# Kernel optimization log

Measured on AMD Instinct MI355X. Metric: run time of the kernel, lower is better.

## Reference

```python
import jax, jax.numpy as jnp
import numpy as np

B, T = 64, 2048
DEC, ENC, ATT, LOC, K = 1024, 512, 128, 32, 31


def setup_inputs() -> dict:
    key = jax.random.key(0)
    ks = jax.random.split(key, 9)
    inv = lambda n: 1.0 / np.sqrt(n)
    return {
        "query": jax.random.normal(ks[0], (B, DEC), dtype=jnp.float32),
        "values": jax.random.normal(ks[1], (B, T, ENC), dtype=jnp.float32),
        "cumulative_attention_weights": jax.random.uniform(ks[2], (B, T), dtype=jnp.float32),
        "mask": jnp.zeros((B, T), dtype=bool),
        "Q_w": jax.random.uniform(ks[3], (ATT, DEC), jnp.float32, -inv(DEC), inv(DEC)),
        "Q_b": jax.random.uniform(ks[4], (ATT,), jnp.float32, -inv(DEC), inv(DEC)),
        "V_w": jax.random.uniform(ks[5], (ATT, ENC), jnp.float32, -inv(ENC), inv(ENC)),
        "conv_w": jax.random.uniform(ks[6], (LOC, 1, K), jnp.float32, -inv(K), inv(K)),
        "loc_proj_w": jax.random.uniform(ks[7], (ATT, LOC), jnp.float32, -inv(LOC), inv(LOC)),
        "v_w": jax.random.uniform(ks[8], (1, ATT), jnp.float32, -inv(ATT), inv(ATT)),
    }


def reference(query, values, cumulative_attention_weights, mask,
              Q_w, Q_b, V_w, conv_w, loc_proj_w, v_w):
    # query projection: [B, 1, ATT] (broadcast over T)
    q = query @ Q_w.T + Q_b                       # [B, ATT]
    q = q[:, None, :]
    # values cache: [B, T, ATT]
    v_cache = jnp.einsum("bte,ae->bta", values, V_w)
    # location features: Conv1d(1 -> LOC, k=31, same padding) over cum weights
    x = cumulative_attention_weights[:, None, :]   # [B, 1, T]
    loc = jax.lax.conv_general_dilated(
        x, conv_w, window_strides=(1,), padding="SAME",
        dimension_numbers=("NCH", "OIH", "NCH"))   # [B, LOC, T]
    loc = jnp.einsum("bct,ac->bta", loc, loc_proj_w)  # [B, T, ATT]
    # additive attention energies
    energies = jnp.tanh(q + v_cache + loc) @ v_w[0]   # [B, T]
    energies = jnp.where(mask, -jnp.inf, energies)
    attention_weights = jax.nn.softmax(energies, axis=1)
    # context: [B, ENC]
    attention_context = jnp.einsum("bt,bte->be", attention_weights, values)
    return attention_context, attention_weights
```

## Files before the change

kernel.cpp:

```cpp
#include <hip/hip_runtime.h>
#include <hip/hip_bf16.h>
#include <math.h>

#define B_  64
#define T_  2048
#define DEC_ 1024
#define ENC_ 512
#define ATT_ 128
#define LOC_ 32
#define KW_  31

typedef __attribute__((ext_vector_type(8))) short short8;
typedef __attribute__((ext_vector_type(4))) float f32x4;
typedef __attribute__((ext_vector_type(4))) unsigned int u32x4;

__device__ inline unsigned short bf16_rn(float x) {
    unsigned int u = __builtin_bit_cast(unsigned int, x);
    unsigned int r = u + 0x7fffu + ((u >> 16) & 1u);
    return (unsigned short)(r >> 16);
}
__device__ inline float bf16_to_f(unsigned short h) {
    unsigned int u = ((unsigned int)h) << 16;
    return __builtin_bit_cast(float, u);
}

__device__ inline void cvt_split8_exact(const float* f, short8& hi8, short8& lo8) {
    u32x4 hw, lw;
    #pragma unroll
    for (int p = 0; p < 4; ++p) {
        float a = f[2 * p], b2 = f[2 * p + 1];
        unsigned u0 = __builtin_bit_cast(unsigned, a);
        unsigned u1 = __builtin_bit_cast(unsigned, b2);
        unsigned r0 = u0 + 0x7fffu + ((u0 >> 16) & 1u);
        unsigned r1 = u1 + 0x7fffu + ((u1 >> 16) & 1u);
        hw[p] = (r0 >> 16) | (r1 & 0xffff0000u);
        float d0 = a  - __builtin_bit_cast(float, r0 & 0xffff0000u);
        float d1 = b2 - __builtin_bit_cast(float, r1 & 0xffff0000u);
        unsigned v0 = __builtin_bit_cast(unsigned, d0);
        unsigned v1 = __builtin_bit_cast(unsigned, d1);
        unsigned s0 = v0 + 0x7fffu + ((v0 >> 16) & 1u);
        unsigned s1 = v1 + 0x7fffu + ((v1 >> 16) & 1u);
        lw[p] = (s0 >> 16) | (s1 & 0xffff0000u);
    }
    hi8 = __builtin_bit_cast(short8, hw);
    lo8 = __builtin_bit_cast(short8, lw);
}

__global__ __launch_bounds__(256) void prep_kernel(
    const float* __restrict__ query, const float* __restrict__ Q_w,
    const float* __restrict__ Q_b, const float* __restrict__ conv_w,
    const float* __restrict__ loc_proj_w, const float* __restrict__ V_w,
    float* __restrict__ qbuf, unsigned short* __restrict__ Bpk,
    unsigned short* __restrict__ effh, unsigned short* __restrict__ effl)
{
    int bi = blockIdx.x, tid = threadIdx.x;
    if (bi < 256) {
        int b = bi >> 2, grp = bi & 3;
        __shared__ float sq[DEC_];
        *(float4*)(&sq[tid * 4]) = *(const float4*)(query + (size_t)b * DEC_ + tid * 4);
        __syncthreads();
        int w = tid >> 6, lane = tid & 63;
        int a0 = grp * 32 + w * 8;
        for (int p = 0; p < 4; ++p) {
            int a = a0 + 2 * p;
            const float* r0 = Q_w + (size_t)a * DEC_;
            const float* r1 = r0 + DEC_;
            float s0 = 0.f, s1 = 0.f;
            #pragma unroll
            for (int i = 0; i < 4; ++i) {
                float4 q0 = *(const float4*)(r0 + i * 256 + lane * 4);
                float4 q1 = *(const float4*)(r1 + i * 256 + lane * 4);
                float4 xq = *(const float4*)(sq + i * 256 + lane * 4);
                s0 += q0.x * xq.x + q0.y * xq.y + q0.z * xq.z + q0.w * xq.w;
                s1 += q1.x * xq.x + q1.y * xq.y + q1.z * xq.z + q1.w * xq.w;
            }
            #pragma unroll
            for (int m = 32; m >= 1; m >>= 1) {
                s0 += __shfl_xor(s0, m, 64);
                s1 += __shfl_xor(s1, m, 64);
            }
            if (lane == 0) {
                qbuf[b * ATT_ + a]     = s0 + Q_b[a];
                qbuf[b * ATT_ + a + 1] = s1 + Q_b[a + 1];
            }
        }
    } else if (bi == 256) {
        __shared__ float slp[ATT_ * LOC_];
        __shared__ float scw[LOC_ * KW_];
        for (int i = tid; i < ATT_ * LOC_; i += 256) slp[i] = loc_proj_w[i];
        for (int i = tid; i < LOC_ * KW_; i += 256) scw[i] = conv_w[i];
        __syncthreads();
        if (tid < ATT_) {
            int n = tid;
            for (int k = 0; k < 32; ++k) {
                float s = 0.f;
                if (k < KW_)
                    #pragma unroll
                    for (int c = 0; c < LOC_; ++c)
                        s += slp[n * LOC_ + c] * scw[c * KW_ + k];
                unsigned short h = bf16_rn(s);
                effh[n * 32 + k] = h;
                effl[n * 32 + k] = bf16_rn(s - bf16_to_f(h));
            }
        }
    } else {
        int g0 = (bi - 257) * 512;
        #pragma unroll
        for (int p = 0; p < 2; ++p) {
            int gi = g0 + p * 256 + tid;
            int n  = gi >> 7;
            int kq = (gi & 127) * 4;
            float4 v = ((const float4*)V_w)[gi];
            ushort4 h4, l4;
            h4.x = bf16_rn(v.x); l4.x = bf16_rn(v.x - bf16_to_f(h4.x));
            h4.y = bf16_rn(v.y); l4.y = bf16_rn(v.y - bf16_to_f(h4.y));
            h4.z = bf16_rn(v.z); l4.z = bf16_rn(v.z - bf16_to_f(h4.z));
            h4.w = bf16_rn(v.w); l4.w = bf16_rn(v.w - bf16_to_f(h4.w));
            int c = kq >> 5;
            int j = n >> 7 == 0 ? (n >> 4) : (n >> 4);
            int l = ((kq & 31) >> 3) * 16 + (n & 15);
            int e = kq & 7;
            int dst = c * 8192 + (n >> 4) * 512 + l * 8 + e;
            (void)j;
            *(ushort4*)(Bpk + dst)        = h4;
            *(ushort4*)(Bpk + dst + 4096) = l4;
        }
    }
}

__global__ __launch_bounds__(256, 2) void energy_ctx_kernel(
    const float* __restrict__ values, const float* __restrict__ cum,
    const float* __restrict__ qbuf, const unsigned short* __restrict__ Bpk,
    const unsigned short* __restrict__ effh, const unsigned short* __restrict__ effl,
    const float* __restrict__ vw, const unsigned char* __restrict__ mask,
    float* __restrict__ wU, float* __restrict__ bstats,
    float* __restrict__ ctxpart)
{
    __shared__ unsigned short sB[2][8192];
    __shared__ float sx[160];
    __shared__ float se[128];
    __shared__ float red[512];

    const int tid = threadIdx.x;
    const int bx  = blockIdx.x;
    const int b   = bx >> 4;
    const int t0  = (bx & 15) * 128;

    if (tid < 160) {
        int g = t0 - 15 + tid;
        sx[tid] = (g >= 0 && g < T_) ? cum[b * T_ + g] : 0.f;
    }
    __syncthreads();

    const int w      = tid >> 6;
    const int lane   = tid & 63;
    const int lane15 = lane & 15;
    const int quad   = lane >> 4;

    f32x4 acc[2][8];
    #pragma unroll
    for (int i = 0; i < 2; ++i)
        #pragma unroll
        for (int j = 0; j < 8; ++j) acc[i][j] = (f32x4){0.f, 0.f, 0.f, 0.f};

    const float* abase = values + ((size_t)b * T_ + t0 + w * 32 + lane15) * ENC_ + quad * 8;

    auto stageB = [&](int buf, int c) {
        const unsigned short* src = Bpk + c * 8192 + w * 512 + lane * 8;
        #pragma unroll
        for (int r = 0; r < 4; ++r) {
            __builtin_amdgcn_global_load_lds(
                (const __attribute__((address_space(1))) unsigned int*)(src + r * 2048),
                (__attribute__((address_space(3))) unsigned int*)(&sB[buf][r * 2048 + w * 512]),
                16, 0, 0);
        }
    };

    float4 pf[2][2];
    stageB(0, 0);
    __builtin_amdgcn_sched_barrier(0);
    #pragma unroll
    for (int i = 0; i < 2; ++i) {
        pf[i][0] = *(const float4*)(abase + i * 16 * ENC_);
        pf[i][1] = *(const float4*)(abase + i * 16 * ENC_ + 4);
    }
    __builtin_amdgcn_sched_barrier(0);
    asm volatile("s_waitcnt vmcnt(4)");
    __builtin_amdgcn_sched_barrier(0);
    __builtin_amdgcn_s_barrier();

    int cur = 0;
    for (int c = 0; c < 16; ++c) {
        if (c + 1 < 16) stageB(cur ^ 1, c + 1);
        __builtin_amdgcn_sched_barrier(0);

        short8 ah[2], al[2];
        #pragma unroll
        for (int i = 0; i < 2; ++i) {
            float fb[8] = {pf[i][0].x, pf[i][0].y, pf[i][0].z, pf[i][0].w,
                           pf[i][1].x, pf[i][1].y, pf[i][1].z, pf[i][1].w};
            cvt_split8_exact(fb, ah[i], al[i]);
        }
        if (c + 1 < 16) {
            int kc = (c + 1) * 32;
            #pragma unroll
            for (int i = 0; i < 2; ++i) {
                pf[i][0] = *(const float4*)(abase + i * 16 * ENC_ + kc);
                pf[i][1] = *(const float4*)(abase + i * 16 * ENC_ + kc + 4);
            }
        }

        #pragma unroll
        for (int j = 0; j < 8; ++j) {
            short8 bh = *(const short8*)&sB[cur][j * 512 + lane * 8];
            short8 bl = *(const short8*)&sB[cur][4096 + j * 512 + lane * 8];
            #pragma unroll
            for (int i = 0; i < 2; ++i) {
                acc[i][j] = __builtin_amdgcn_mfma_f32_16x16x32_bf16(ah[i], bh, acc[i][j], 0, 0, 0);
                acc[i][j] = __builtin_amdgcn_mfma_f32_16x16x32_bf16(ah[i], bl, acc[i][j], 0, 0, 0);
                acc[i][j] = __builtin_amdgcn_mfma_f32_16x16x32_bf16(al[i], bh, acc[i][j], 0, 0, 0);
            }
        }

        if (c + 1 < 16) {
            __builtin_amdgcn_sched_barrier(0);
            asm volatile("s_waitcnt vmcnt(4)");
            __builtin_amdgcn_sched_barrier(0);
            __builtin_amdgcn_s_barrier();
            cur ^= 1;
        }
    }

    {
        short8 ah[2], al[2];
        #pragma unroll
        for (int i = 0; i < 2; ++i) {
            int base = w * 32 + i * 16 + lane15 + quad * 8;
            float xv[8];
            #pragma unroll
            for (int j2 = 0; j2 < 8; ++j2) xv[j2] = sx[base + j2];
            cvt_split8_exact(xv, ah[i], al[i]);
        }
        #pragma unroll
        for (int j = 0; j < 8; ++j) {
            int n = j * 16 + lane15;
            short8 bh = *(const short8*)(effh + n * 32 + quad * 8);
            short8 bl = *(const short8*)(effl + n * 32 + quad * 8);
            #pragma unroll
            for (int i = 0; i < 2; ++i) {
                acc[i][j] = __builtin_amdgcn_mfma_f32_16x16x32_bf16(ah[i], bh, acc[i][j], 0, 0, 0);
                acc[i][j] = __builtin_amdgcn_mfma_f32_16x16x32_bf16(ah[i], bl, acc[i][j], 0, 0, 0);
                acc[i][j] = __builtin_amdgcn_mfma_f32_16x16x32_bf16(al[i], bh, acc[i][j], 0, 0, 0);
            }
        }
    }

    float qv[8], vv[8];
    #pragma unroll
    for (int j = 0; j < 8; ++j) {
        int n = j * 16 + lane15;
        qv[j] = qbuf[b * ATT_ + n];
        vv[j] = vw[n];
    }
    #pragma unroll
    for (int i = 0; i < 2; ++i)
        #pragma unroll
        for (int r = 0; r < 4; ++r) {
            float s = 0.f;
            #pragma unroll
            for (int j = 0; j < 8; ++j)
                s += vv[j] * tanhf(acc[i][j][r] + qv[j]);
            #pragma unroll
            for (int m = 8; m >= 1; m >>= 1) s += __shfl_xor(s, m, 64);
            if (lane15 == 0)
                se[w * 32 + i * 16 + quad * 4 + r] = s;
        }
    __syncthreads();

    if (tid < 128 && mask[b * T_ + t0 + tid]) se[tid] = -INFINITY;
    __syncthreads();

    float e0 = se[lane * 2], e1 = se[lane * 2 + 1];
    float mx = fmaxf(e0, e1);
    #pragma unroll
    for (int m = 32; m >= 1; m >>= 1) mx = fmaxf(mx, __shfl_xor(mx, m, 64));
    float w0 = 0.f, w1 = 0.f;
    if (mx > -INFINITY) {
        w0 = expf(e0 - mx);
        w1 = expf(e1 - mx);
    }
    float sm = w0 + w1;
    #pragma unroll
    for (int m = 32; m >= 1; m >>= 1) sm += __shfl_xor(sm, m, 64);
    __syncthreads();

    if (w == 0) {
        se[lane * 2]     = w0;
        se[lane * 2 + 1] = w1;
        *(float2*)(wU + b * T_ + t0 + lane * 2) = make_float2(w0, w1);
        if (lane == 0)
            *(float2*)(bstats + bx * 2) = make_float2(mx, sm);
    }
    __syncthreads();

    {
        int tt = tid >> 7;
        int e4 = (tid & 127) * 4;
        const float* vp = values + ((size_t)b * T_ + t0 + tt * 64) * ENC_ + e4;
        float4 cacc = make_float4(0.f, 0.f, 0.f, 0.f);
        #pragma unroll 8
        for (int t = 0; t < 64; ++t) {
            float4 v = *(const float4*)(vp + (size_t)t * ENC_);
            float wv = se[tt * 64 + t];
            cacc.x += wv * v.x; cacc.y += wv * v.y;
            cacc.z += wv * v.z; cacc.w += wv * v.w;
        }
        if (tt == 1) *(float4*)&red[e4] = cacc;
        __syncthreads();
        if (tt == 0) {
            float4 o = *(const float4*)&red[e4];
            float4 tot = make_float4(cacc.x + o.x, cacc.y + o.y,
                                     cacc.z + o.z, cacc.w + o.w);
            *(float4*)(ctxpart + (size_t)bx * ENC_ + e4) = tot;
        }
    }
}

__global__ __launch_bounds__(256) void combine_kernel(
    const float* __restrict__ bstats, const float* __restrict__ ctxpart,
    const float* __restrict__ wU, float* __restrict__ out)
{
    int b = blockIdx.x, tid = threadIdx.x;
    __shared__ float smx[16], ssm[16], ssc[16];
    if (tid < 16) {
        float2 st = *(const float2*)(bstats + (b * 16 + tid) * 2);
        smx[tid] = st.x; ssm[tid] = st.y;
    }
    __syncthreads();
    float M = -INFINITY;
    #pragma unroll
    for (int k = 0; k < 16; ++k) M = fmaxf(M, smx[k]);
    if (tid < 16)
        ssc[tid] = (smx[tid] > -INFINITY) ? expf(smx[tid] - M) : 0.f;
    __syncthreads();
    float S = 0.f;
    #pragma unroll
    for (int k = 0; k < 16; ++k) S += ssm[k] * ssc[k];
    float invS = 1.f / S;

    float* ctx  = out;
    float* wout = out + B_ * ENC_;

    float cx = 0.f, cy = 0.f;
    #pragma unroll
    for (int k = 0; k < 16; ++k) {
        float2 v = *(const float2*)(ctxpart + (size_t)(b * 16 + k) * ENC_ + tid * 2);
        cx += v.x * ssc[k]; cy += v.y * ssc[k];
    }
    *(float2*)(ctx + b * ENC_ + tid * 2) = make_float2(cx * invS, cy * invS);

    #pragma unroll
    for (int p = 0; p < 8; ++p) {
        int t = p * 256 + tid;
        wout[b * T_ + t] = wU[b * T_ + t] * ssc[t >> 7] * invS;
    }
}

extern "C" void kernel_launch(void* const* d_in, const int* in_sizes, int n_in,
                              void* d_out, int out_size, void* d_ws, size_t ws_size,
                              hipStream_t stream) {
    const float* query        = (const float*)d_in[0];
    const float* values       = (const float*)d_in[1];
    const float* cum          = (const float*)d_in[2];
    const unsigned char* mask = (const unsigned char*)d_in[3];
    const float* Q_w          = (const float*)d_in[4];
    const float* Q_b          = (const float*)d_in[5];
    const float* V_w          = (const float*)d_in[6];
    const float* conv_w       = (const float*)d_in[7];
    const float* loc_proj_w   = (const float*)d_in[8];
    const float* v_w          = (const float*)d_in[9];

    float* out = (float*)d_out;
    char*  ws  = (char*)d_ws;
    float*          qbuf     = (float*)(ws);
    unsigned short* Bpk      = (unsigned short*)(ws + 32768);
    unsigned short* effh     = (unsigned short*)(ws + 294912);
    unsigned short* effl     = (unsigned short*)(ws + 303104);
    float*          wU       = (float*)(ws + 311296);
    float*          bstats   = (float*)(ws + 835584);
    float*          ctxpart  = (float*)(ws + 843776);

    prep_kernel<<<289, 256, 0, stream>>>(query, Q_w, Q_b, conv_w, loc_proj_w, V_w,
                                         qbuf, Bpk, effh, effl);
    energy_ctx_kernel<<<1024, 256, 0, stream>>>(values, cum, qbuf, Bpk,
                                                effh, effl, v_w, mask,
                                                wU, bstats, ctxpart);
    combine_kernel<<<B_, 256, 0, stream>>>(bstats, ctxpart, wU, out);
}
```

Before: 460.3 us.

## Deepen GEMM pipeline to triple-buffered LDS and two-stage register prefetch

The value-projection GEMM loop now stages weight chunks two iterations ahead in a three-slot LDS ring and keeps two register sets of prefetched fp32 activation loads in flight. The loop is fully unrolled so buffer indices are compile-time constants, and the vmcnt waits are adjusted to the deeper queue. Launch bounds are raised to request three blocks per CU. This is meant to hide global memory latency on the streaming values read, at the cost of more LDS (48 KB for sB) and more registers, which may prevent the targeted occupancy or cause spills.

```diff
diff --git a/kernel.cpp b/kernel.cpp
--- a/kernel.cpp
+++ b/kernel.cpp
@@ -117,18 +117,16 @@
             h4.z = bf16_rn(v.z); l4.z = bf16_rn(v.z - bf16_to_f(h4.z));
             h4.w = bf16_rn(v.w); l4.w = bf16_rn(v.w - bf16_to_f(h4.w));
             int c = kq >> 5;
-            int j = n >> 7 == 0 ? (n >> 4) : (n >> 4);
             int l = ((kq & 31) >> 3) * 16 + (n & 15);
             int e = kq & 7;
             int dst = c * 8192 + (n >> 4) * 512 + l * 8 + e;
-            (void)j;
             *(ushort4*)(Bpk + dst)        = h4;
             *(ushort4*)(Bpk + dst + 4096) = l4;
         }
     }
 }
 
-__global__ __launch_bounds__(256, 2) void energy_ctx_kernel(
+__global__ __launch_bounds__(256, 3) void energy_ctx_kernel(
     const float* __restrict__ values, const float* __restrict__ cum,
     const float* __restrict__ qbuf, const unsigned short* __restrict__ Bpk,
     const unsigned short* __restrict__ effh, const unsigned short* __restrict__ effl,
@@ -136,7 +134,7 @@
     float* __restrict__ wU, float* __restrict__ bstats,
     float* __restrict__ ctxpart)
 {
-    __shared__ unsigned short sB[2][8192];
+    __shared__ unsigned short sB[3][8192];
     __shared__ float sx[160];
     __shared__ float se[128];
     __shared__ float red[512];
@@ -175,45 +173,48 @@
                 16, 0, 0);
         }
     };
-
-    float4 pf[2][2];
+    float4 pf[2][2][2];
+    auto issueA = [&](float4 (&pfX)[2][2], int kc) {
+        #pragma unroll
+        for (int i = 0; i < 2; ++i) {
+            pfX[i][0] = *(const float4*)(abase + i * 16 * ENC_ + kc);
+            pfX[i][1] = *(const float4*)(abase + i * 16 * ENC_ + kc + 4);
+        }
+    };
+
     stageB(0, 0);
+    stageB(1, 1);
     __builtin_amdgcn_sched_barrier(0);
-    #pragma unroll
-    for (int i = 0; i < 2; ++i) {
-        pf[i][0] = *(const float4*)(abase + i * 16 * ENC_);
-        pf[i][1] = *(const float4*)(abase + i * 16 * ENC_ + 4);
-    }
+    issueA(pf[0], 0);
+    issueA(pf[1], 32);
     __builtin_amdgcn_sched_barrier(0);
-    asm volatile("s_waitcnt vmcnt(4)");
+    asm volatile("s_waitcnt vmcnt(12)");
     __builtin_amdgcn_sched_barrier(0);
     __builtin_amdgcn_s_barrier();
 
-    int cur = 0;
+    #pragma unroll
     for (int c = 0; c < 16; ++c) {
-        if (c + 1 < 16) stageB(cur ^ 1, c + 1);
+        if (c + 2 < 16) stageB((c + 2) % 3, c + 2);
         __builtin_amdgcn_sched_barrier(0);
 
         short8 ah[2], al[2];
         #pragma unroll
         for (int i = 0; i < 2; ++i) {
-            float fb[8] = {pf[i][0].x, pf[i][0].y, pf[i][0].z, pf[i][0].w,
-                           pf[i][1].x, pf[i][1].y, pf[i][1].z, pf[i][1].w};
+            float fb[8] = {pf[c & 1][i][0].x, pf[c & 1][i][0].y,
+                           pf[c & 1][i][0].z, pf[c & 1][i][0].w,
+                           pf[c & 1][i][1].x, pf[c & 1][i][1].y,
+                           pf[c & 1][i][1].z, pf[c & 1][i][1].w};
             cvt_split8_exact(fb, ah[i], al[i]);
         }
-        if (c + 1 < 16) {
-            int kc = (c + 1) * 32;
-            #pragma unroll
-            for (int i = 0; i < 2; ++i) {
-                pf[i][0] = *(const float4*)(abase + i * 16 * ENC_ + kc);
-                pf[i][1] = *(const float4*)(abase + i * 16 * ENC_ + kc + 4);
-            }
-        }
+        __builtin_amdgcn_sched_barrier(0);
+
+        if (c + 2 < 16) issueA(pf[c & 1], (c + 2) * 32);
+        __builtin_amdgcn_sched_barrier(0);
 
         #pragma unroll
         for (int j = 0; j < 8; ++j) {
-            short8 bh = *(const short8*)&sB[cur][j * 512 + lane * 8];
-            short8 bl = *(const short8*)&sB[cur][4096 + j * 512 + lane * 8];
+            short8 bh = *(const short8*)&sB[c % 3][j * 512 + lane * 8];
+            short8 bl = *(const short8*)&sB[c % 3][4096 + j * 512 + lane * 8];
             #pragma unroll
             for (int i = 0; i < 2; ++i) {
                 acc[i][j] = __builtin_amdgcn_mfma_f32_16x16x32_bf16(ah[i], bh, acc[i][j], 0, 0, 0);
@@ -222,12 +223,12 @@
             }
         }
 
-        if (c + 1 < 16) {
+        if (c < 15) {
             __builtin_amdgcn_sched_barrier(0);
-            asm volatile("s_waitcnt vmcnt(4)");
+            if (c + 2 < 16) asm volatile("s_waitcnt vmcnt(12)");
+            else            asm volatile("s_waitcnt vmcnt(4)");
             __builtin_amdgcn_sched_barrier(0);
             __builtin_amdgcn_s_barrier();
-            cur ^= 1;
         }
     }
 
```

Measured after the change: 462.0 us. No clear change (+0.4%).
